# Kernel optimization log

Measured on AMD Instinct MI355X. Metric: run time of the kernel, lower is better.

The kernel has to match this reference:

```python
import jax, jax.numpy as jnp
import numpy as np

V = 96103   # pegasus-xsum vocab
D = 1024    # d_model
H = 16      # heads
DH = D // H
F = 4096    # ffn
L = 2       # enc and dec layers (reduced from 16 for the reference)
S = 512     # source length
T = 80      # max_length
B = 4       # batch of sources
NS = 5      # num_return_sequences
BN = B * NS # decode streams
TOPK = 100
EOS = 1
MINLEN = 7
EMB_SCALE = float(np.sqrt(D))


def ln(x):
    m = jnp.mean(x, -1, keepdims=True)
    v = jnp.mean((x - m) ** 2, -1, keepdims=True)
    return (x - m) * jax.lax.rsqrt(v + 1e-5)


def setup_inputs() -> dict:
    key = jax.random.key(0)
    ks = jax.random.split(key, 16)
    g = lambda k, s: (jax.random.normal(k, s) * 0.02).astype(jnp.float32)
    return {
        "ids": jax.random.randint(ks[0], (B, S), 0, 96000).astype(jnp.int32),
        "mask": jnp.ones((B, S), jnp.int32),
        "E": g(ks[1], (V, D)),
        "pos_e": g(ks[2], (S, D)),
        "pos_d": g(ks[3], (T, D)),
        "enc_attn_in": g(ks[4], (L, D, 3 * D)),
        "enc_attn_out": g(ks[5], (L, D, D)),
        "enc_ffn1": g(ks[6], (L, D, F)),
        "enc_ffn2": g(ks[7], (L, F, D)),
        "dec_sa_in": g(ks[8], (L, D, 3 * D)),
        "dec_sa_out": g(ks[9], (L, D, D)),
        "dec_ca_q": g(ks[10], (L, D, D)),
        "dec_ca_kv": g(ks[11], (L, D, 2 * D)),
        "dec_ca_out": g(ks[12], (L, D, D)),
        "dec_ffn1": g(ks[13], (L, D, F)),
        "dec_ffn2": g(ks[14], (L, F, D)),
    }


def _generate(ids, mask, E, pos_e, pos_d, enc_attn_in, enc_attn_out, enc_ffn1,
              enc_ffn2, dec_sa_in, dec_sa_out, dec_ca_q, dec_ca_kv, dec_ca_out,
              dec_ffn1, dec_ffn2):
    inv = 1.0 / float(np.sqrt(DH))
    # ---------------- encoder ----------------
    x = E[ids] * EMB_SCALE + pos_e[None]                       # [B,S,D]
    bias = (1.0 - mask.astype(jnp.float32))[:, None, None, :] * -1e9  # [B,1,1,S]
    for l in range(L):
        h = ln(x)
        qkv = h @ enc_attn_in[l]
        q = qkv[..., :D].reshape(B, S, H, DH)
        k = qkv[..., D:2 * D].reshape(B, S, H, DH)
        v = qkv[..., 2 * D:].reshape(B, S, H, DH)
        sc = jnp.einsum('bqhd,bkhd->bhqk', q, k) * inv + bias
        a = jnp.einsum('bhqk,bkhd->bqhd', jax.nn.softmax(sc, -1), v).reshape(B, S, D)
        x = x + a @ enc_attn_out[l]
        h = ln(x)
        x = x + jax.nn.gelu(h @ enc_ffn1[l]) @ enc_ffn2[l]
    enc = ln(x)
    # expand to BN = B * num_return_sequences decode streams
    enc_r = jnp.repeat(enc, NS, axis=0)                        # [BN,S,D]
    bias_r = jnp.repeat(bias, NS, axis=0)[:, :, 0, :]          # [BN,1,S]
    # precompute cross-attn K/V per decoder layer
    ckv = jnp.einsum('bsd,lde->lbse', enc_r, dec_ca_kv)        # [L,BN,S,2D]
    cK = ckv[..., :D].reshape(L, BN, S, H, DH)
    cV = ckv[..., D:].reshape(L, BN, S, H, DH)

    key_base = jax.random.key(1234)
    cache_k0 = jnp.zeros((L, BN, T, H, DH), jnp.float32)
    cache_v0 = jnp.zeros((L, BN, T, H, DH), jnp.float32)

    def step(carry, t):
        ck, cv, prev = carry
        x = E[prev] * EMB_SCALE + pos_d[t]                     # [BN,D]
        for l in range(L):
            h = ln(x)
            qkv = h @ dec_sa_in[l]
            q = qkv[:, :D].reshape(BN, H, DH)
            k = qkv[:, D:2 * D].reshape(BN, H, DH)
            v = qkv[:, 2 * D:].reshape(BN, H, DH)
            ck = ck.at[l, :, t].set(k)
            cv = cv.at[l, :, t].set(v)
            sc = jnp.einsum('bhd,bkhd->bhk', q, ck[l]) * inv
            sc = sc + jnp.where(jnp.arange(T) <= t, 0.0, -1e9)
            a = jnp.einsum('bhk,bkhd->bhd', jax.nn.softmax(sc, -1), cv[l]).reshape(BN, D)
            x = x + a @ dec_sa_out[l]
            h = ln(x)
            q2 = (h @ dec_ca_q[l]).reshape(BN, H, DH)
            sc2 = jnp.einsum('bhd,bshd->bhs', q2, cK[l]) * inv + bias_r
            a2 = jnp.einsum('bhs,bshd->bhd', jax.nn.softmax(sc2, -1), cV[l]).reshape(BN, D)
            x = x + a2 @ dec_ca_out[l]
            h = ln(x)
            x = x + jax.nn.gelu(h @ dec_ffn1[l]) @ dec_ffn2[l]
        x = ln(x)
        logits = x @ E.T                                       # [BN,V]
        forbid = (t < MINLEN - 1) & (jnp.arange(V) == EOS)     # min_length: block EOS
        logits = jnp.where(forbid, -1e9, logits)
        topv, topi = jax.lax.top_k(logits, TOPK)               # top_k=100 sampling
        sel = jax.random.categorical(jax.random.fold_in(key_base, t), topv)
        tok = jnp.take_along_axis(topi, sel[:, None], 1)[:, 0]
        lp = jnp.take_along_axis(jax.nn.log_softmax(logits, -1), tok[:, None], 1)[:, 0]
        return (ck, cv, tok), (tok, lp)

    init = (cache_k0, cache_v0, jnp.zeros((BN,), jnp.int32))  # start token = pad(0)
    _, (toks, lps) = jax.lax.scan(step, init, jnp.arange(T))
    return toks.T, lps.T                                       # [BN,T] each


def reference(ids, mask, E, pos_e, pos_d, enc_attn_in, enc_attn_out, enc_ffn1,
              enc_ffn2, dec_sa_in, dec_sa_out, dec_ca_q, dec_ca_kv, dec_ca_out,
              dec_ffn1, dec_ffn2):
    toks, _ = _generate(ids, mask, E, pos_e, pos_d, enc_attn_in, enc_attn_out,
                        enc_ffn1, enc_ffn2, dec_sa_in, dec_sa_out, dec_ca_q,
                        dec_ca_kv, dec_ca_out, dec_ffn1, dec_ffn2)
    # matches the torch module: [batch, num_seq, max_len] token ids
    return toks.reshape(B, NS, T)
```

## Files before the change

kernel.cpp:

```cpp
#include <hip/hip_runtime.h>
#include <cstdint>
#include <cstddef>

#define DEV __device__ __forceinline__

constexpr int V  = 96103;
constexpr int VPAD = 96104;
constexpr int D  = 1024;
constexpr int H  = 16;
constexpr int DH = 64;
constexpr int F  = 4096;
constexpr int NL = 2;
constexpr int S  = 512;
constexpr int T  = 80;
constexpr int B  = 4;
constexpr int NS = 5;
constexpr int BN = 20;
constexpr int KTOP = 100;
constexpr int EOS = 1;
constexpr int LCOLS = 188;
constexpr int LGRID = (V + LCOLS - 1) / LCOLS;


DEV float gelu_f(float x) {
  float x3 = x * x * x;
  float inner = 0.7978845608028654f * (x + 0.044715f * x3);
  float tt = tanhf(inner);
  return x * (0.5f * (1.0f + tt));
}

DEV void tf2x32(unsigned k0, unsigned k1, unsigned& x0, unsigned& x1) {
  unsigned ks2 = k0 ^ k1 ^ 0x1BD11BDAu;
#define TFR(rr) { x0 += x1; x1 = (x1 << rr) | (x1 >> (32 - rr)); x1 ^= x0; }
  x0 += k0; x1 += k1;
  TFR(13) TFR(15) TFR(26) TFR(6)
  x0 += k1;  x1 += ks2 + 1u;
  TFR(17) TFR(29) TFR(16) TFR(24)
  x0 += ks2; x1 += k0 + 2u;
  TFR(13) TFR(15) TFR(26) TFR(6)
  x0 += k0;  x1 += k1 + 3u;
  TFR(17) TFR(29) TFR(16) TFR(24)
  x0 += k1;  x1 += ks2 + 4u;
  TFR(13) TFR(15) TFR(26) TFR(6)
  x0 += ks2; x1 += k0 + 5u;
#undef TFR
}

DEV unsigned long long sort_key(float v, unsigned idx) {
  unsigned bb = __float_as_uint(v);
  bb = (bb & 0x80000000u) ? ~bb : (bb | 0x80000000u);
  return ((unsigned long long)bb << 32) | (unsigned long long)(0xFFFFFFFFu - idx);
}

template<int NWAVE>
DEV void ln_to_lds(const float* __restrict__ x, float* xs, int tid) {
  int w = tid >> 6, lane = tid & 63;
  for (int m = w; m < BN; m += NWAVE) {
    float4 v[4];
    float sum = 0.0f;
#pragma unroll
    for (int j = 0; j < 4; ++j) {
      v[j] = *(const float4*)(x + m * D + j * 256 + lane * 4);
      sum += v[j].x + v[j].y + v[j].z + v[j].w;
    }
#pragma unroll
    for (int o = 32; o > 0; o >>= 1) sum += __shfl_xor(sum, o);
    float mean = sum * (1.0f / 1024.0f);
    float vs = 0.0f;
#pragma unroll
    for (int j = 0; j < 4; ++j) {
      float a = v[j].x - mean, b = v[j].y - mean, c = v[j].z - mean, d = v[j].w - mean;
      vs += a * a + b * b + c * c + d * d;
    }
#pragma unroll
    for (int o = 32; o > 0; o >>= 1) vs += __shfl_xor(vs, o);
    float rsig = 1.0f / sqrtf(vs * (1.0f / 1024.0f) + 1e-5f);
#pragma unroll
    for (int j = 0; j < 4; ++j) {
      float4 ov;
      ov.x = (v[j].x - mean) * rsig; ov.y = (v[j].y - mean) * rsig;
      ov.z = (v[j].z - mean) * rsig; ov.w = (v[j].w - mean) * rsig;
      *(float4*)(xs + m * D + j * 256 + lane * 4) = ov;
    }
  }
}

DEV void row_ln_stats(const float* __restrict__ xd, int bn, float* xrow,
                      float* wred, float& rstd, float& bco, int tid) {
  int w = tid >> 6, lane = tid & 63;
  float4 v = *(const float4*)(xd + (size_t)bn * D + w * 256 + lane * 4);
  *(float4*)(xrow + w * 256 + lane * 4) = v;
  float s = v.x + v.y + v.z + v.w;
#pragma unroll
  for (int o = 32; o > 0; o >>= 1) s += __shfl_xor(s, o);
  if (lane == 0) wred[w] = s;
  __syncthreads();
  float mean = (wred[0] + wred[1] + wred[2] + wred[3]) * (1.0f / 1024.0f);
  float a = v.x - mean, b = v.y - mean, c = v.z - mean, d = v.w - mean;
  float s2 = a * a + b * b + c * c + d * d;
#pragma unroll
  for (int o = 32; o > 0; o >>= 1) s2 += __shfl_xor(s2, o);
  if (lane == 0) wred[4 + w] = s2;
  __syncthreads();
  rstd = 1.0f / sqrtf((wred[4] + wred[5] + wred[6] + wred[7]) * (1.0f / 1024.0f) + 1e-5f);
  bco = -mean * rstd;
}


__global__ __launch_bounds__(256) void embed_enc(const int* __restrict__ ids,
                                                 const float* __restrict__ E,
                                                 const float* __restrict__ pos_e,
                                                 float* __restrict__ xe) {
  int row = blockIdx.x;
  int id = ids[row];
  const float* er = E + (size_t)id * D;
  const float* pr = pos_e + (size_t)(row % S) * D;
  float* xr = xe + (size_t)row * D;
  for (int j = threadIdx.x; j < D; j += 256)
    xr[j] = er[j] * 32.0f + pr[j];
}

__global__ __launch_bounds__(256) void embed_dec(const float* __restrict__ E,
                                                 const float* __restrict__ pos_d,
                                                 const int* __restrict__ toks,
                                                 float* __restrict__ xd, int t) {
  int bn = blockIdx.x;
  int prev = (t == 0) ? 0 : toks[bn * T + (t - 1)];
  const float* er = E + (size_t)prev * D;
  const float* pr = pos_d + (size_t)t * D;
  float* xr = xd + (size_t)bn * D;
  for (int j = threadIdx.x; j < D; j += 256)
    xr[j] = er[j] * 32.0f + pr[j];
}


__global__ __launch_bounds__(256) void ln_kernel(const float* __restrict__ x,
                                                 float* __restrict__ y) {
  __shared__ float red[256];
  __shared__ float sv[2];
  int tid = threadIdx.x;
  const float* xr = x + (size_t)blockIdx.x * D;
  float4 v = *(const float4*)(xr + tid * 4);
  red[tid] = v.x + v.y + v.z + v.w;
  __syncthreads();
  for (int k = 128; k > 0; k >>= 1) { if (tid < k) red[tid] += red[tid + k]; __syncthreads(); }
  if (tid == 0) sv[0] = red[0] * (1.0f / 1024.0f);
  __syncthreads();
  float m = sv[0];
  float dx = v.x - m, dy = v.y - m, dz = v.z - m, dw = v.w - m;
  red[tid] = dx * dx + dy * dy + dz * dz + dw * dw;
  __syncthreads();
  for (int k = 128; k > 0; k >>= 1) { if (tid < k) red[tid] += red[tid + k]; __syncthreads(); }
  if (tid == 0) sv[1] = 1.0f / sqrtf(red[0] * (1.0f / 1024.0f) + 1e-5f);
  __syncthreads();
  float r = sv[1];
  float* yr = y + (size_t)blockIdx.x * D;
  float4 o; o.x = dx * r; o.y = dy * r; o.z = dz * r; o.w = dw * r;
  *(float4*)(yr + tid * 4) = o;
}


template<int EPI>
__global__ __launch_bounds__(256) void gemm128(const float* __restrict__ A,
                                               const float* __restrict__ W,
                                               const float* X, float* C,
                                               int Kd, int Nd) {
  __shared__ __align__(16) float As[8][128];
  __shared__ __align__(16) float Bs[8][128];
  int tid = threadIdx.x;
  int n0 = blockIdx.x * 128, m0 = blockIdx.y * 128;
  int tx = tid & 15, ty = tid >> 4;
  int ar = tid >> 1, ac = (tid & 1) * 4;
  int br = tid >> 5, bc = (tid & 31) * 4;
  float acc[8][8] = {};
  for (int k0 = 0; k0 < Kd; k0 += 8) {
    float4 av = *(const float4*)(A + (size_t)(m0 + ar) * Kd + k0 + ac);
    float4 wv = *(const float4*)(W + (size_t)(k0 + br) * Nd + n0 + bc);
    __syncthreads();
    As[ac + 0][ar] = av.x; As[ac + 1][ar] = av.y;
    As[ac + 2][ar] = av.z; As[ac + 3][ar] = av.w;
    *(float4*)&Bs[br][bc] = wv;
    __syncthreads();
#pragma unroll
    for (int k = 0; k < 8; ++k) {
      float a8[8], b8[8];
      *(float4*)&a8[0] = *(const float4*)&As[k][ty * 8];
      *(float4*)&a8[4] = *(const float4*)&As[k][ty * 8 + 4];
      *(float4*)&b8[0] = *(const float4*)&Bs[k][tx * 8];
      *(float4*)&b8[4] = *(const float4*)&Bs[k][tx * 8 + 4];
#pragma unroll
      for (int i = 0; i < 8; ++i)
#pragma unroll
        for (int j = 0; j < 8; ++j)
          acc[i][j] = fmaf(a8[i], b8[j], acc[i][j]);
    }
  }
#pragma unroll
  for (int i = 0; i < 8; ++i) {
    int m = m0 + ty * 8 + i;
#pragma unroll
    for (int j = 0; j < 8; ++j) {
      int n = n0 + tx * 8 + j;
      float r = acc[i][j];
      size_t off = (size_t)m * Nd + n;
      if (EPI == 1) r = X[off] + r;
      if (EPI == 2) r = gelu_f(r);
      C[off] = r;
    }
  }
}


__global__ __launch_bounds__(256) void enc_attn(const float* __restrict__ qkv,
                                                const int* __restrict__ mask,
                                                float* __restrict__ ab) {
  __shared__ __align__(16) float qv[64];
  __shared__ float sc[512];
  __shared__ float red[256];
  __shared__ float sv[2];
  int tid = threadIdx.x;
  int q = blockIdx.x % S;
  int h = (blockIdx.x / S) % H;
  int b = blockIdx.x / (S * H);
  const float* qrow = qkv + (size_t)(b * S + q) * (3 * D) + h * 64;
  if (tid < 64) qv[tid] = qrow[tid];
  __syncthreads();
  float lmax = -INFINITY;
  for (int k = tid; k < S; k += 256) {
    const float* kr = qkv + (size_t)(b * S + k) * (3 * D) + D + h * 64;
    float dot = 0.0f;
#pragma unroll
    for (int d4 = 0; d4 < 16; ++d4) {
      float4 kk = *(const float4*)(kr + d4 * 4);
      float4 qq = *(const float4*)(qv + d4 * 4);
      dot += qq.x * kk.x + qq.y * kk.y + qq.z * kk.z + qq.w * kk.w;
    }
    float bias = (1.0f - (float)mask[b * S + k]) * -1e9f;
    float val = dot * 0.125f + bias;
    sc[k] = val;
    lmax = fmaxf(lmax, val);
  }
  red[tid] = lmax; __syncthreads();
  for (int k = 128; k > 0; k >>= 1) { if (tid < k) red[tid] = fmaxf(red[tid], red[tid + k]); __syncthreads(); }
  if (tid == 0) sv[0] = red[0];
  __syncthreads();
  float mx = sv[0];
  float lsum = 0.0f;
  for (int k = tid; k < S; k += 256) { float e = expf(sc[k] - mx); sc[k] = e; lsum += e; }
  red[tid] = lsum; __syncthreads();
  for (int k = 128; k > 0; k >>= 1) { if (tid < k) red[tid] += red[tid + k]; __syncthreads(); }
  if (tid == 0) sv[1] = red[0];
  __syncthreads();
  float den = sv[1];
  for (int k = tid; k < S; k += 256) sc[k] = sc[k] / den;
  __syncthreads();
  int d = tid & 63, c = tid >> 6;
  const float* vb = qkv + (size_t)(b * S) * (3 * D) + 2 * D + h * 64 + d;
  float part = 0.0f;
  for (int k = c * 128; k < c * 128 + 128; ++k)
    part = fmaf(sc[k], vb[(size_t)k * (3 * D)], part);
  red[tid] = part; __syncthreads();
  if (tid < 64) {
    float o = red[tid] + red[tid + 64] + red[tid + 128] + red[tid + 192];
    ab[(size_t)(b * S + q) * D + h * 64 + tid] = o;
  }
}


template<int CT, int EPI, bool KV, bool LNIN>
__global__ __launch_bounds__(512) void dec_gemm(const float* __restrict__ x,
                                                const float* __restrict__ W,
                                                const float* Xres, float* Cout,
                                                float* __restrict__ cacheK,
                                                float* __restrict__ cacheV,
                                                int Kd, int Nd, int t, int l) {
  constexpr int KSP = 512 / CT;
  __shared__ float red[CT * 20 * (KSP + 1)];
  __shared__ float redw[CT * (KSP + 1)];
  __shared__ float sab[40];
  int tid = threadIdx.x;
  if constexpr (LNIN) {
    int w = tid >> 6, lane = tid & 63;
    for (int m = w; m < BN; m += 8) {
      const float* xr = x + (size_t)m * 1024 + lane * 16;
      float4 v[4];
      float sum = 0.0f;
#pragma unroll
      for (int j = 0; j < 4; ++j) {
        v[j] = *(const float4*)(xr + j * 4);
        sum += v[j].x + v[j].y + v[j].z + v[j].w;
      }
#pragma unroll
      for (int o = 32; o > 0; o >>= 1) sum += __shfl_xor(sum, o);
      float mean = sum * (1.0f / 1024.0f);
      float vs = 0.0f;
#pragma unroll
      for (int j = 0; j < 4; ++j) {
        float a = v[j].x - mean, b = v[j].y - mean, c2 = v[j].z - mean, d = v[j].w - mean;
        vs += a * a + b * b + c2 * c2 + d * d;
      }
#pragma unroll
      for (int o = 32; o > 0; o >>= 1) vs += __shfl_xor(vs, o);
      float rstd = 1.0f / sqrtf(vs * (1.0f / 1024.0f) + 1e-5f);
      if (lane == 0) { sab[m] = rstd; sab[20 + m] = -mean * rstd; }
    }
    __syncthreads();
  }
  int c = tid % CT, ks = tid / CT;
  int klen = Kd / KSP;
  const float* Wp = W + (size_t)(ks * klen) * Nd + blockIdx.x * CT + c;
  float acc[20] = {};
  float accw = 0.0f;
  for (int kk = 0; kk < klen; kk += 8) {
    float wv[8];
#pragma unroll
    for (int u = 0; u < 8; ++u) wv[u] = Wp[(size_t)u * Nd];
    Wp += (size_t)8 * Nd;
    if constexpr (LNIN)
      accw += wv[0] + wv[1] + wv[2] + wv[3] + wv[4] + wv[5] + wv[6] + wv[7];
    int kb = ks * klen + kk;
#pragma unroll
    for (int m = 0; m < 20; ++m) {
      float4 x0 = *(const float4*)(x + (size_t)m * Kd + kb);
      float4 x1 = *(const float4*)(x + (size_t)m * Kd + kb + 4);
      float a = acc[m];
      a = fmaf(x0.x, wv[0], a); a = fmaf(x0.y, wv[1], a);
      a = fmaf(x0.z, wv[2], a); a = fmaf(x0.w, wv[3], a);
      a = fmaf(x1.x, wv[4], a); a = fmaf(x1.y, wv[5], a);
      a = fmaf(x1.z, wv[6], a); a = fmaf(x1.w, wv[7], a);
      acc[m] = a;
    }
  }
#pragma unroll
  for (int m = 0; m < 20; ++m) red[(c * 20 + m) * (KSP + 1) + ks] = acc[m];
  if constexpr (LNIN) redw[c * (KSP + 1) + ks] = accw;
  __syncthreads();
  if (tid < CT * 20) {
    int cc = tid % CT, m = tid / CT;
    const float* rp = red + (cc * 20 + m) * (KSP + 1);
    float s = 0.0f;
#pragma unroll
    for (int k2 = 0; k2 < KSP; ++k2) s += rp[k2];
    if constexpr (LNIN) {
      const float* rw = redw + cc * (KSP + 1);
      float sw = 0.0f;
#pragma unroll
      for (int k2 = 0; k2 < KSP; ++k2) sw += rw[k2];
      s = sab[m] * s + sab[20 + m] * sw;
    }
    int ng = blockIdx.x * CT + cc;
    if constexpr (KV) {
      if (ng < D) {
        Cout[(size_t)m * Nd + ng] = s;
      } else if (ng < 2 * D) {
        cacheK[(((size_t)l * BN + m) * T + t) * D + (ng - D)] = s;
      } else {
        cacheV[(((size_t)l * BN + m) * T + t) * D + (ng - 2 * D)] = s;
      }
    } else {
      size_t off = (size_t)m * Nd + ng;
      if (EPI == 1) s = Xres[off] + s;
      if (EPI == 2) s = gelu_f(s);
      Cout[off] = s;
    }
  }
}


__global__ __launch_bounds__(256) void qkv_selfattn2(const float* __restrict__ xd,
                                                     const float* __restrict__ Wqkv,
                                                     const float* __restrict__ Wso,
                                                     float* __restrict__ cacheK,
                                                     float* __restrict__ cacheV,
                                                     float* __restrict__ part1,
                                                     int t, int l) {
  __shared__ __align__(16) float xrow[1024];
  __shared__ __align__(16) float qv[64], kt[64], vt[64], ov[64];
  __shared__ float sc[96];
  __shared__ float wred[8];
  __shared__ float sv[2];
  int tid = threadIdx.x;
  int h = blockIdx.x / BN, bn = blockIdx.x % BN;
  float rstd, bco;
  row_ln_stats(xd, bn, xrow, wred, rstd, bco, tid);
  __syncthreads();
  if (tid < 192) {
    int part = tid >> 6;
    int c = tid & 63;
    const float* Wp = Wqkv + (size_t)part * D + (size_t)h * 64 + c;
    float acc = 0.0f, accw = 0.0f;
    for (int k = 0; k < 1024; k += 8) {
      float wv[8];
#pragma unroll
      for (int u = 0; u < 8; ++u) wv[u] = Wp[(size_t)(k + u) * (3 * D)];
#pragma unroll
      for (int u = 0; u < 8; ++u) {
        acc = fmaf(xrow[k + u], wv[u], acc);
        accw += wv[u];
      }
    }
    float val = rstd * acc + bco * accw;
    if (part == 0) {
      qv[c] = val;
    } else if (part == 1) {
      kt[c] = val;
      cacheK[(((size_t)l * BN + bn) * T + t) * D + h * 64 + c] = val;
    } else {
      vt[c] = val;
      cacheV[(((size_t)l * BN + bn) * T + t) * D + h * 64 + c] = val;
    }
  }
  __syncthreads();
  int n = t + 1;
  if (tid < t) {
    const float* kr = cacheK + (((size_t)l * BN + bn) * T + tid) * D + h * 64;
    float dot = 0.0f;
#pragma unroll
    for (int d4 = 0; d4 < 16; ++d4) {
      float4 kk = *(const float4*)(kr + d4 * 4);
      float4 qq = *(const float4*)(qv + d4 * 4);
      dot += qq.x * kk.x + qq.y * kk.y + qq.z * kk.z + qq.w * kk.w;
    }
    sc[tid] = dot * 0.125f;
  } else if (tid == t) {
    float dot = 0.0f;
#pragma unroll
    for (int d4 = 0; d4 < 16; ++d4) {
      float4 kk = *(const float4*)(kt + d4 * 4);
      float4 qq = *(const float4*)(qv + d4 * 4);
      dot += qq.x * kk.x + qq.y * kk.y + qq.z * kk.z + qq.w * kk.w;
    }
    sc[t] = dot * 0.125f;
  }
  __syncthreads();
  if (tid == 0) {
    float mx = -INFINITY;
    for (int k = 0; k < n; ++k) mx = fmaxf(mx, sc[k]);
    sv[0] = mx;
  }
  __syncthreads();
  if (tid < n) sc[tid] = expf(sc[tid] - sv[0]);
  __syncthreads();
  if (tid == 0) {
    float s = 0.0f;
    for (int k = 0; k < n; ++k) s += sc[k];
    sv[1] = s;
  }
  __syncthreads();
  if (tid < n) sc[tid] = sc[tid] / sv[1];
  __syncthreads();
  if (tid < 64) {
    const float* vb = cacheV + ((size_t)l * BN + bn) * T * D + h * 64 + tid;
    float o = 0.0f;
    for (int k = 0; k < t; ++k) o = fmaf(sc[k], vb[(size_t)k * D], o);
    o = fmaf(sc[t], vt[tid], o);
    ov[tid] = o;
  }
  __syncthreads();
  {
    int c0 = tid * 4;
    const float* wbase = Wso + (size_t)(h * 64) * D + c0;
    float4 a = {0.0f, 0.0f, 0.0f, 0.0f};
    for (int j = 0; j < 64; ++j) {
      float oj = ov[j];
      float4 wr = *(const float4*)(wbase + (size_t)j * D);
      a.x = fmaf(oj, wr.x, a.x); a.y = fmaf(oj, wr.y, a.y);
      a.z = fmaf(oj, wr.z, a.z); a.w = fmaf(oj, wr.w, a.w);
    }
    *(float4*)(part1 + ((size_t)h * BN + bn) * D + c0) = a;
  }
}


__global__ __launch_bounds__(256) void caq_crossattn2(const float* __restrict__ xd,
                                                      const float* __restrict__ part1,
                                                      const float* __restrict__ Wcq,
                                                      const float* __restrict__ cKVl,
                                                      const int* __restrict__ mask,
                                                      float* __restrict__ y,
                                                      float* __restrict__ ad) {
  __shared__ __align__(16) float xrow[1024];
  __shared__ __align__(16) float qv[64];
  __shared__ float sc[512];
  __shared__ float red[256];
  __shared__ float qred[256], qredw[256];
  __shared__ float wred[8];
  __shared__ float sv[2];
  int tid = threadIdx.x;
  int h = blockIdx.x / BN, bn = blockIdx.x % BN;
  int b = bn / NS;
  int w = tid >> 6, lane = tid & 63;
  int c0 = tid * 4;
  float4 r = *(const float4*)(xd + (size_t)bn * D + c0);
  for (int hh = 0; hh < H; ++hh) {
    float4 p = *(const float4*)(part1 + ((size_t)hh * BN + bn) * D + c0);
    r.x += p.x; r.y += p.y; r.z += p.z; r.w += p.w;
  }
  *(float4*)(xrow + c0) = r;
  if (h == 0) *(float4*)(y + (size_t)bn * D + c0) = r;
  float s = r.x + r.y + r.z + r.w;
#pragma unroll
  for (int o = 32; o > 0; o >>= 1) s += __shfl_xor(s, o);
  if (lane == 0) wred[w] = s;
  __syncthreads();
  float mean = (wred[0] + wred[1] + wred[2] + wred[3]) * (1.0f / 1024.0f);
  float da = r.x - mean, db = r.y - mean, dc = r.z - mean, dd = r.w - mean;
  float s2 = da * da + db * db + dc * dc + dd * dd;
#pragma unroll
  for (int o = 32; o > 0; o >>= 1) s2 += __shfl_xor(s2, o);
  if (lane == 0) wred[4 + w] = s2;
  __syncthreads();
  float rstd = 1.0f / sqrtf((wred[4] + wred[5] + wred[6] + wred[7]) * (1.0f / 1024.0f) + 1e-5f);
  float bco = -mean * rstd;
  {
    int c = tid & 63, ks = tid >> 6;
    const float* Wp = Wcq + (size_t)(ks * 256) * D + (size_t)h * 64 + c;
    float acc = 0.0f, accw = 0.0f;
    for (int k = 0; k < 256; k += 8) {
      float wv[8];
#pragma unroll
      for (int u = 0; u < 8; ++u) wv[u] = Wp[(size_t)(k + u) * D];
#pragma unroll
      for (int u = 0; u < 8; ++u) {
        acc = fmaf(xrow[ks * 256 + k + u], wv[u], acc);
        accw += wv[u];
      }
    }
    qred[ks * 64 + c] = acc;
    qredw[ks * 64 + c] = accw;
  }
  __syncthreads();
  if (tid < 64) {
    float a = qred[tid] + qred[64 + tid] + qred[128 + tid] + qred[192 + tid];
    float aw = qredw[tid] + qredw[64 + tid] + qredw[128 + tid] + qredw[192 + tid];
    qv[tid] = rstd * a + bco * aw;
  }
  __syncthreads();
  const float* base = cKVl + (size_t)b * S * (2 * D);
  float lmax = -INFINITY;
  for (int s3 = tid; s3 < S; s3 += 256) {
    const float* kr = base + (size_t)s3 * (2 * D) + h * 64;
    float dot = 0.0f;
#pragma unroll
    for (int d4 = 0; d4 < 16; ++d4) {
      float4 kk = *(const float4*)(kr + d4 * 4);
      float4 qq = *(const float4*)(qv + d4 * 4);
      dot += qq.x * kk.x + qq.y * kk.y + qq.z * kk.z + qq.w * kk.w;
    }
    float bias = (1.0f - (float)mask[b * S + s3]) * -1e9f;
    float val = dot * 0.125f + bias;
    sc[s3] = val;
    lmax = fmaxf(lmax, val);
  }
  red[tid] = lmax; __syncthreads();
  for (int k = 128; k > 0; k >>= 1) { if (tid < k) red[tid] = fmaxf(red[tid], red[tid + k]); __syncthreads(); }
  if (tid == 0) sv[0] = red[0];
  __syncthreads();
  float mx = sv[0];
  float lsum = 0.0f;
  for (int s3 = tid; s3 < S; s3 += 256) { float e = expf(sc[s3] - mx); sc[s3] = e; lsum += e; }
  red[tid] = lsum; __syncthreads();
  for (int k = 128; k > 0; k >>= 1) { if (tid < k) red[tid] += red[tid + k]; __syncthreads(); }
  if (tid == 0) sv[1] = red[0];
  __syncthreads();
  float den = sv[1];
  for (int s3 = tid; s3 < S; s3 += 256) sc[s3] = sc[s3] / den;
  __syncthreads();
  int d = tid & 63, c = tid >> 6;
  const float* vb = base + D + h * 64 + d;
  float part = 0.0f;
  for (int s3 = c * 128; s3 < c * 128 + 128; ++s3)
    part = fmaf(sc[s3], vb[(size_t)s3 * (2 * D)], part);
  red[tid] = part; __syncthreads();
  if (tid < 64) {
    float o = red[tid] + red[tid + 64] + red[tid + 128] + red[tid + 192];
    ad[(size_t)bn * D + h * 64 + tid] = o;
  }
}


__global__ __launch_bounds__(256) void logits3(const float* __restrict__ xd,
                                               const float* __restrict__ E,
                                               float* __restrict__ logits) {
  __shared__ float xs[20 * 1024];
  int tid = threadIdx.x;
  ln_to_lds<4>(xd, xs, tid);
  __syncthreads();
  int n = blockIdx.x * LCOLS + tid;
  if (tid < LCOLS && n < V) {
    const float* er = E + (size_t)n * D;
    float acc[20] = {};
    for (int k = 0; k < 1024; k += 8) {
      float4 e0 = *(const float4*)(er + k);
      float4 e1 = *(const float4*)(er + k + 4);
#pragma unroll
      for (int m = 0; m < 20; ++m) {
        const float* xb = xs + m * 1024 + k;
        float4 x0 = *(const float4*)(xb);
        float4 x1 = *(const float4*)(xb + 4);
        float a = acc[m];
        a = fmaf(x0.x, e0.x, a); a = fmaf(x0.y, e0.y, a);
        a = fmaf(x0.z, e0.z, a); a = fmaf(x0.w, e0.w, a);
        a = fmaf(x1.x, e1.x, a); a = fmaf(x1.y, e1.y, a);
        a = fmaf(x1.z, e1.z, a); a = fmaf(x1.w, e1.w, a);
        acc[m] = a;
      }
    }
#pragma unroll
    for (int m = 0; m < 20; ++m)
      logits[(size_t)m * VPAD + n] = acc[m];
  } else if (n == V) {
#pragma unroll
    for (int m = 0; m < 20; ++m)
      logits[(size_t)m * VPAD + V] = -1e30f;
  }
}


__global__ __launch_bounds__(256) void topk_sample(const float* __restrict__ logits,
                                                   int* __restrict__ toks,
                                                   const float* __restrict__ E,
                                                   const float* __restrict__ pos_d,
                                                   float* __restrict__ xd, int t) {
  __shared__ unsigned long long keys[2048];
  __shared__ float svals[128];
  __shared__ unsigned sidx[128];
  __shared__ int stok;
  int tid = threadIdx.x;
  int bn = blockIdx.x;
  const float* row = logits + (size_t)bn * VPAD;

  float tv[8]; unsigned ti[8];
#pragma unroll
  for (int j = 0; j < 8; ++j) { tv[j] = -INFINITY; ti[j] = 0xFFFFFFFFu; }

  for (int i4 = tid * 4; i4 < VPAD; i4 += 1024) {
    float4 v4 = *(const float4*)(row + i4);
    float vv[4] = {v4.x, v4.y, v4.z, v4.w};
#pragma unroll
    for (int j = 0; j < 4; ++j) {
      int i = i4 + j;
      float v = vv[j];
      if (t < 6 && i == EOS) v = -1e9f;
      if (v > tv[7]) {
        tv[7] = v; ti[7] = (unsigned)i;
#pragma unroll
        for (int jj = 7; jj > 0; --jj) {
          if (tv[jj] > tv[jj - 1]) {
            float a = tv[jj]; tv[jj] = tv[jj - 1]; tv[jj - 1] = a;
            unsigned bi = ti[jj]; ti[jj] = ti[jj - 1]; ti[jj - 1] = bi;
          }
        }
      }
    }
  }
#pragma unroll
  for (int j = 0; j < 8; ++j) keys[tid * 8 + j] = ~sort_key(tv[j], ti[j]);
  __syncthreads();

  for (int ksz = 2; ksz <= 2048; ksz <<= 1) {
    for (int jj = ksz >> 1; jj > 0; jj >>= 1) {
      for (int i = tid; i < 2048; i += 256) {
        int ixj = i ^ jj;
        if (ixj > i) {
          unsigned long long a = keys[i], b2 = keys[ixj];
          bool up = ((i & ksz) == 0);
          if ((a > b2) == up) { keys[i] = b2; keys[ixj] = a; }
        }
      }
      __syncthreads();
    }
  }

  if (tid < KTOP) {
    unsigned long long kk = ~keys[tid];
    unsigned sb = (unsigned)(kk >> 32);
    unsigned idx = 0xFFFFFFFFu - (unsigned)(kk & 0xFFFFFFFFull);
    unsigned fb = (sb & 0x80000000u) ? (sb ^ 0x80000000u) : ~sb;
    float v = __uint_as_float(fb);
    unsigned a0 = 0u, a1 = (unsigned)t;
    tf2x32(0u, 1234u, a0, a1);
    unsigned c0 = 0u, c1 = (unsigned)(bn * KTOP + tid);
    tf2x32(a0, a1, c0, c1);
    unsigned bits = c0 ^ c1;
    float f = __uint_as_float((bits >> 9) | 0x3f800000u) - 1.0f;
    float u = fmaxf(f, 1.17549435e-38f);
    float g = -logf(-logf(u));
    svals[tid] = v + g;
    sidx[tid] = idx;
  }
  __syncthreads();
  if (tid == 0) {
    int best = 0; float bv = svals[0];
    for (int j = 1; j < KTOP; ++j) { if (svals[j] > bv) { bv = svals[j]; best = j; } }
    int tok = (int)sidx[best];
    toks[bn * T + t] = tok;
    stok = tok;
  }
  __syncthreads();
  if (t + 1 < T) {
    int tok = stok;
    const float* er = E + (size_t)tok * D;
    const float* pr = pos_d + (size_t)(t + 1) * D;
    for (int j = tid; j < D; j += 256)
      xd[(size_t)bn * D + j] = er[j] * 32.0f + pr[j];
  }
}


extern "C" void kernel_launch(void* const* d_in, const int* in_sizes, int n_in,
                              void* d_out, int out_size, void* d_ws, size_t ws_size,
                              hipStream_t stream) {
  (void)in_sizes; (void)n_in; (void)out_size; (void)ws_size;

  const int*   ids   = (const int*)d_in[0];
  const int*   maskp = (const int*)d_in[1];
  const float* E     = (const float*)d_in[2];
  const float* pos_e = (const float*)d_in[3];
  const float* pos_d = (const float*)d_in[4];
  const float* eai   = (const float*)d_in[5];
  const float* eao   = (const float*)d_in[6];
  const float* ef1   = (const float*)d_in[7];
  const float* ef2   = (const float*)d_in[8];
  const float* dsi   = (const float*)d_in[9];
  const float* dso   = (const float*)d_in[10];
  const float* dcq   = (const float*)d_in[11];
  const float* dckv  = (const float*)d_in[12];
  const float* dco   = (const float*)d_in[13];
  const float* df1   = (const float*)d_in[14];
  const float* df2   = (const float*)d_in[15];

  float* ws = (float*)d_ws;
  size_t o = 0;
  auto alloc = [&](size_t n) { size_t r = o; o += (n + 63) & ~(size_t)63; return r; };
  float* cKV    = ws + alloc((size_t)NL * B * S * 2 * D);
  float* cacheK = ws + alloc((size_t)NL * BN * T * D);
  float* cacheV = ws + alloc((size_t)NL * BN * T * D);
  float* xe     = ws + alloc((size_t)B * S * D);
  float* he     = ws + alloc((size_t)B * S * D);
  float* qkvb   = ws + alloc((size_t)B * S * 3 * D);
  float* ab     = ws + alloc((size_t)B * S * D);
  float* ffb    = ws + alloc((size_t)B * S * F);
  float* xd      = qkvb;
  float* ad      = xd + BN * D;
  float* yb      = ad + BN * D;
  float* y2b     = yb + BN * D;
  float* ffd     = y2b + BN * D;
  float* part1   = ffd + BN * F;
  float* logitsb = part1 + H * BN * D;
  int* toks = (int*)d_out;

  embed_enc<<<B * S, 256, 0, stream>>>(ids, E, pos_e, xe);
  for (int l = 0; l < NL; ++l) {
    ln_kernel<<<B * S, 256, 0, stream>>>(xe, he);
    gemm128<0><<<dim3(3 * D / 128, B * S / 128), 256, 0, stream>>>(
        he, eai + (size_t)l * D * 3 * D, nullptr, qkvb, D, 3 * D);
    enc_attn<<<B * H * S, 256, 0, stream>>>(qkvb, maskp, ab);
    gemm128<1><<<dim3(D / 128, B * S / 128), 256, 0, stream>>>(
        ab, eao + (size_t)l * D * D, xe, xe, D, D);
    ln_kernel<<<B * S, 256, 0, stream>>>(xe, he);
    gemm128<2><<<dim3(F / 128, B * S / 128), 256, 0, stream>>>(
        he, ef1 + (size_t)l * D * F, nullptr, ffb, D, F);
    gemm128<1><<<dim3(D / 128, B * S / 128), 256, 0, stream>>>(
        ffb, ef2 + (size_t)l * F * D, xe, xe, F, D);
  }
  ln_kernel<<<B * S, 256, 0, stream>>>(xe, he);
  for (int l = 0; l < NL; ++l) {
    gemm128<0><<<dim3(2 * D / 128, B * S / 128), 256, 0, stream>>>(
        he, dckv + (size_t)l * D * 2 * D, nullptr,
        cKV + (size_t)l * B * S * 2 * D, D, 2 * D);
  }

  embed_dec<<<BN, 256, 0, stream>>>(E, pos_d, toks, xd, 0);
  for (int t = 0; t < T; ++t) {
    for (int l = 0; l < NL; ++l) {
      qkv_selfattn2<<<H * BN, 256, 0, stream>>>(
          xd, dsi + (size_t)l * D * 3 * D, dso + (size_t)l * D * D,
          cacheK, cacheV, part1, t, l);
      caq_crossattn2<<<H * BN, 256, 0, stream>>>(
          xd, part1, dcq + (size_t)l * D * D,
          cKV + (size_t)l * B * S * 2 * D, maskp, yb, ad);
      dec_gemm<8, 1, false, false><<<D / 8, 512, 0, stream>>>(
          ad, dco + (size_t)l * D * D, yb, y2b, nullptr, nullptr, D, D, 0, 0);
      dec_gemm<16, 2, false, true><<<F / 16, 512, 0, stream>>>(
          y2b, df1 + (size_t)l * D * F, nullptr, ffd, nullptr, nullptr, D, F, 0, 0);
      dec_gemm<8, 1, false, false><<<D / 8, 512, 0, stream>>>(
          ffd, df2 + (size_t)l * F * D, y2b, xd, nullptr, nullptr, F, D, 0, 0);
    }
    logits3<<<LGRID, 256, 0, stream>>>(xd, E, logitsb);
    topk_sample<<<BN, 256, 0, stream>>>(logitsb, toks, E, pos_d, xd, t);
  }
}
```

Measured before the change: 54.09 ms.

## Fold layernorm into logits via row stats and split-K across thread halves

```diff
diff --git a/kernel.cpp b/kernel.cpp
--- a/kernel.cpp
+++ b/kernel.cpp
@@ -18,8 +18,8 @@
 constexpr int BN = 20;
 constexpr int KTOP = 100;
 constexpr int EOS = 1;
-constexpr int LCOLS = 188;
-constexpr int LGRID = (V + LCOLS - 1) / LCOLS;
+constexpr int L5C = 128;
+constexpr int L5GRID = (V + L5C - 1) / L5C;
 
 
 DEV float gelu_f(float x) {
@@ -50,39 +50,6 @@
   unsigned bb = __float_as_uint(v);
   bb = (bb & 0x80000000u) ? ~bb : (bb | 0x80000000u);
   return ((unsigned long long)bb << 32) | (unsigned long long)(0xFFFFFFFFu - idx);
-}
-
-template<int NWAVE>
-DEV void ln_to_lds(const float* __restrict__ x, float* xs, int tid) {
-  int w = tid >> 6, lane = tid & 63;
-  for (int m = w; m < BN; m += NWAVE) {
-    float4 v[4];
-    float sum = 0.0f;
-#pragma unroll
-    for (int j = 0; j < 4; ++j) {
-      v[j] = *(const float4*)(x + m * D + j * 256 + lane * 4);
-      sum += v[j].x + v[j].y + v[j].z + v[j].w;
-    }
-#pragma unroll
-    for (int o = 32; o > 0; o >>= 1) sum += __shfl_xor(sum, o);
-    float mean = sum * (1.0f / 1024.0f);
-    float vs = 0.0f;
-#pragma unroll
-    for (int j = 0; j < 4; ++j) {
-      float a = v[j].x - mean, b = v[j].y - mean, c = v[j].z - mean, d = v[j].w - mean;
-      vs += a * a + b * b + c * c + d * d;
-    }
-#pragma unroll
-    for (int o = 32; o > 0; o >>= 1) vs += __shfl_xor(vs, o);
-    float rsig = 1.0f / sqrtf(vs * (1.0f / 1024.0f) + 1e-5f);
-#pragma unroll
-    for (int j = 0; j < 4; ++j) {
-      float4 ov;
-      ov.x = (v[j].x - mean) * rsig; ov.y = (v[j].y - mean) * rsig;
-      ov.z = (v[j].z - mean) * rsig; ov.w = (v[j].w - mean) * rsig;
-      *(float4*)(xs + m * D + j * 256 + lane * 4) = ov;
-    }
-  }
 }
 
 DEV void row_ln_stats(const float* __restrict__ xd, int bn, float* xrow,
@@ -579,40 +546,82 @@
 }
 
 
-__global__ __launch_bounds__(256) void logits3(const float* __restrict__ xd,
+__global__ __launch_bounds__(256) void logits5(const float* __restrict__ xd,
                                                const float* __restrict__ E,
                                                float* __restrict__ logits) {
-  __shared__ float xs[20 * 1024];
+  __shared__ float sab[40];
+  __shared__ float reda[20][L5C];
+  __shared__ float redw[L5C];
   int tid = threadIdx.x;
-  ln_to_lds<4>(xd, xs, tid);
-  __syncthreads();
-  int n = blockIdx.x * LCOLS + tid;
-  if (tid < LCOLS && n < V) {
-    const float* er = E + (size_t)n * D;
-    float acc[20] = {};
-    for (int k = 0; k < 1024; k += 8) {
-      float4 e0 = *(const float4*)(er + k);
-      float4 e1 = *(const float4*)(er + k + 4);
+  {
+    int w = tid >> 6, lane = tid & 63;
+    for (int m = w; m < BN; m += 4) {
+      const float* xr = xd + (size_t)m * D + lane * 16;
+      float4 v[4];
+      float sum = 0.0f;
+#pragma unroll
+      for (int j = 0; j < 4; ++j) {
+        v[j] = *(const float4*)(xr + j * 4);
+        sum += v[j].x + v[j].y + v[j].z + v[j].w;
+      }
+#pragma unroll
+      for (int o = 32; o > 0; o >>= 1) sum += __shfl_xor(sum, o);
+      float mean = sum * (1.0f / 1024.0f);
+      float vs = 0.0f;
+#pragma unroll
+      for (int j = 0; j < 4; ++j) {
+        float a = v[j].x - mean, b = v[j].y - mean, c2 = v[j].z - mean, d = v[j].w - mean;
+        vs += a * a + b * b + c2 * c2 + d * d;
+      }
+#pragma unroll
+      for (int o = 32; o > 0; o >>= 1) vs += __shfl_xor(vs, o);
+      float rstd = 1.0f / sqrtf(vs * (1.0f / 1024.0f) + 1e-5f);
+      if (lane == 0) { sab[m] = rstd; sab[20 + m] = -mean * rstd; }
+    }
+  }
+  __syncthreads();
+  int khalf = tid >> 7, col = tid & 127;
+  int n = blockIdx.x * L5C + col;
+  int nc = n < V ? n : V - 1;
+  const float* er = E + (size_t)nc * D + khalf * 512;
+  const float* xb = xd + khalf * 512;
+  float acc[20] = {};
+  float accw = 0.0f;
+  for (int k = 0; k < 512; k += 8) {
+    float4 e0 = *(const float4*)(er + k);
+    float4 e1 = *(const float4*)(er + k + 4);
+    accw += e0.x + e0.y + e0.z + e0.w + e1.x + e1.y + e1.z + e1.w;
+#pragma unroll
+    for (int m = 0; m < 20; ++m) {
+      float4 x0 = *(const float4*)(xb + (size_t)m * D + k);
+      float4 x1 = *(const float4*)(xb + (size_t)m * D + k + 4);
+      float a = acc[m];
+      a = fmaf(x0.x, e0.x, a); a = fmaf(x0.y, e0.y, a);
+      a = fmaf(x0.z, e0.z, a); a = fmaf(x0.w, e0.w, a);
+      a = fmaf(x1.x, e1.x, a); a = fmaf(x1.y, e1.y, a);
+      a = fmaf(x1.z, e1.z, a); a = fmaf(x1.w, e1.w, a);
+      acc[m] = a;
+    }
+  }
+  if (khalf == 1) {
+#pragma unroll
+    for (int m = 0; m < 20; ++m) reda[m][col] = acc[m];
+    redw[col] = accw;
+  }
+  __syncthreads();
+  if (khalf == 0) {
+    if (n < V) {
+      float aw = accw + redw[col];
 #pragma unroll
       for (int m = 0; m < 20; ++m) {
-        const float* xb = xs + m * 1024 + k;
-        float4 x0 = *(const float4*)(xb);
-        float4 x1 = *(const float4*)(xb + 4);
-        float a = acc[m];
-        a = fmaf(x0.x, e0.x, a); a = fmaf(x0.y, e0.y, a);
-        a = fmaf(x0.z, e0.z, a); a = fmaf(x0.w, e0.w, a);
-        a = fmaf(x1.x, e1.x, a); a = fmaf(x1.y, e1.y, a);
-        a = fmaf(x1.z, e1.z, a); a = fmaf(x1.w, e1.w, a);
-        acc[m] = a;
-      }
-    }
-#pragma unroll
-    for (int m = 0; m < 20; ++m)
-      logits[(size_t)m * VPAD + n] = acc[m];
-  } else if (n == V) {
-#pragma unroll
-    for (int m = 0; m < 20; ++m)
-      logits[(size_t)m * VPAD + V] = -1e30f;
+        float s = acc[m] + reda[m][col];
+        logits[(size_t)m * VPAD + n] = sab[m] * s + sab[20 + m] * aw;
+      }
+    } else if (n == V) {
+#pragma unroll
+      for (int m = 0; m < 20; ++m)
+        logits[(size_t)m * VPAD + V] = -1e30f;
+    }
   }
 }
 
@@ -787,7 +796,7 @@
       dec_gemm<8, 1, false, false><<<D / 8, 512, 0, stream>>>(
           ffd, df2 + (size_t)l * F * D, y2b, xd, nullptr, nullptr, F, D, 0, 0);
     }
-    logits3<<<LGRID, 256, 0, stream>>>(xd, E, logitsb);
+    logits5<<<L5GRID, 256, 0, stream>>>(xd, E, logitsb);
     topk_sample<<<BN, 256, 0, stream>>>(logitsb, toks, E, pos_d, xd, t);
   }
 }
```

New measurement: 68.54 ms. 1.27x slower.
